# Kernel tuning notes

Measured on AMD Instinct MI355X. Metric: run time of the kernel, lower is better.

Reference implementation:

```python
import jax, jax.numpy as jnp
import numpy as np

N_NODES = 100000
N_EDGES = 1600000
NFEAT, NHID, NCLASS = 128, 64, 16


def setup_inputs() -> dict:
    key = jax.random.key(0)
    ks = jax.random.split(key, 8)
    x = jax.random.normal(ks[0], (N_NODES, NFEAT), dtype=jnp.float32)
    src = jax.random.randint(ks[1], (N_EDGES,), 0, N_NODES, dtype=jnp.int32)
    dst = jax.random.randint(ks[2], (N_EDGES,), 0, N_NODES, dtype=jnp.int32)
    edge_weight = jax.random.uniform(ks[3], (N_EDGES,), dtype=jnp.float32)
    W1 = jax.random.normal(ks[4], (NFEAT, NHID), dtype=jnp.float32) / np.sqrt(NFEAT)
    b1 = jnp.zeros((NHID,), dtype=jnp.float32)
    W2 = jax.random.normal(ks[5], (NHID, NCLASS), dtype=jnp.float32) / np.sqrt(NHID)
    b2 = jnp.zeros((NCLASS,), dtype=jnp.float32)
    return {"x": x, "src": src, "dst": dst, "edge_weight": edge_weight,
            "W1": W1, "b1": b1, "W2": W2, "b2": b2}


def _spmm(src, dst, edge_weight, support):
    # out[i] = sum_{e: dst[e]==i} w[e] * support[src[e]]   (adj @ support)
    msgs = edge_weight[:, None] * support[src]  # [E, d]
    return jax.ops.segment_sum(msgs, dst, num_segments=N_NODES)


def reference(x, src, dst, edge_weight, W1, b1, W2, b2):
    # layer 1: dense projection then sparse aggregation, relu
    h = jax.nn.relu(_spmm(src, dst, edge_weight, x @ W1) + b1)  # [N, nhid]
    # layer 2: identity activation
    logits = _spmm(src, dst, edge_weight, h @ W2) + b2          # [N, nclass]
    return jax.nn.log_softmax(logits, axis=1)
```

## Files before the change

### kernel.cpp

```cpp
#include <hip/hip_runtime.h>

#define N_NODES 100000
#define N_EDGES 1600000
#define NFEAT 128
#define NHID 64
#define NCLASS 16

#define BSHIFT 7
#define BUCK_NODES 128
#define NBUCK ((N_NODES + BUCK_NODES - 1) >> BSHIFT)
#define ECAP 2560
#define EDGE_TILE 8192
#define NB_SCAT ((N_EDGES + EDGE_TILE - 1) / EDGE_TILE)
#define EPT 16
#define NB_GEMM ((N_NODES + 127) / 128)

#define HPAD 65

#define SCALE1 262144.0f
#define INV_SCALE1 (1.0f / 262144.0f)
#define SCALE2 131072.0f
#define INV_SCALE2 (1.0f / 131072.0f)

typedef __attribute__((ext_vector_type(8))) short short8;
typedef __attribute__((ext_vector_type(4))) float float4v;

__device__ __forceinline__ float bflo(unsigned int u) {
    return __uint_as_float(u << 16);
}
__device__ __forceinline__ float bfhi(unsigned int u) {
    return __uint_as_float(u & 0xFFFF0000u);
}
__device__ __forceinline__ unsigned short f2bf(float f) {
    unsigned int b = __float_as_uint(f);
    b += 0x7FFFu + ((b >> 16) & 1u);
    return (unsigned short)(b >> 16);
}
__device__ __forceinline__ int fx(float v, float scale) {
    return __float2int_rn(v * scale);
}

__global__ __launch_bounds__(512) void k_gemm1_scatter(
        const float* __restrict__ x, const float* __restrict__ W1,
        unsigned short* __restrict__ s1,
        const int* __restrict__ dst, const int* __restrict__ src,
        const float* __restrict__ ew,
        int* __restrict__ fill, int2* __restrict__ edgeA) {
    __shared__ unsigned short w1t[64][136];
    __shared__ int hist[NBUCK], bbase[NBUCK], bfill[NBUCK];

    if (blockIdx.x >= NB_GEMM) {
        for (int i = threadIdx.x; i < NBUCK; i += 512) { hist[i] = 0; bfill[i] = 0; }

        const int bid  = blockIdx.x - NB_GEMM;
        const int base = bid * EDGE_TILE;
        int   d[EPT]; int s[EPT]; float w[EPT]; bool v[EPT];
#pragma unroll
        for (int k = 0; k < EPT; ++k) {
            int e = base + threadIdx.x + k * 512;
            v[k] = e < N_EDGES;
            d[k] = v[k] ? dst[e] : 0;
        }
#pragma unroll
        for (int k = 0; k < EPT; ++k) {
            int e = base + threadIdx.x + k * 512;
            s[k] = v[k] ? src[e] : 0;
        }
#pragma unroll
        for (int k = 0; k < EPT; ++k) {
            int e = base + threadIdx.x + k * 512;
            w[k] = v[k] ? ew[e] : 0.f;
        }
        __syncthreads();

#pragma unroll
        for (int k = 0; k < EPT; ++k)
            if (v[k]) atomicAdd(&hist[d[k] >> BSHIFT], 1);
        __syncthreads();

        {
            int rot = (bid * 53) % NBUCK;
            for (int i = threadIdx.x; i < NBUCK; i += 512) {
                int j = i + rot;
                if (j >= NBUCK) j -= NBUCK;
                bbase[j] = hist[j] ? atomicAdd(&fill[j], hist[j]) : 0;
            }
        }
        __syncthreads();

#pragma unroll
        for (int k = 0; k < EPT; ++k) {
            if (v[k]) {
                int bb = d[k] >> BSHIFT;
                int r  = bbase[bb] + atomicAdd(&bfill[bb], 1);
                if (r < ECAP)
                    edgeA[(size_t)bb * ECAP + r] =
                        make_int2(s[k] | ((d[k] & (BUCK_NODES - 1)) << 17),
                                  __float_as_int(w[k]));
            }
        }
        return;
    }

    for (int i = threadIdx.x; i < NFEAT * NHID; i += 512) {
        int n = i & 63, k = i >> 6;
        w1t[n][k] = f2bf(W1[k * NHID + n]);
    }
    __syncthreads();

    const int lane = threadIdx.x & 63;
    const int wv   = threadIdx.x >> 6;
    const int m    = lane & 15;
    const int quad = lane >> 4;
    const int node0 = blockIdx.x * 128 + wv * 16;
    if (node0 >= N_NODES) return;

    short8 bfrag[4][4];
#pragma unroll
    for (int kt = 0; kt < 4; ++kt)
#pragma unroll
        for (int nt = 0; nt < 4; ++nt)
            bfrag[kt][nt] = *(const short8*)&w1t[nt * 16 + m][kt * 32 + quad * 8];

    const float4* xr = (const float4*)(x + (size_t)node0 * NFEAT);
    float4v acc[4] = {{0.f,0.f,0.f,0.f},{0.f,0.f,0.f,0.f},
                      {0.f,0.f,0.f,0.f},{0.f,0.f,0.f,0.f}};
#pragma unroll
    for (int kt = 0; kt < 4; ++kt) {
        float4 f0 = xr[m * 32 + kt * 8 + quad * 2];
        float4 f1 = xr[m * 32 + kt * 8 + quad * 2 + 1];
        short8 a;
        a[0] = (short)f2bf(f0.x); a[1] = (short)f2bf(f0.y);
        a[2] = (short)f2bf(f0.z); a[3] = (short)f2bf(f0.w);
        a[4] = (short)f2bf(f1.x); a[5] = (short)f2bf(f1.y);
        a[6] = (short)f2bf(f1.z); a[7] = (short)f2bf(f1.w);
#pragma unroll
        for (int nt = 0; nt < 4; ++nt)
            acc[nt] = __builtin_amdgcn_mfma_f32_16x16x32_bf16(
                a, bfrag[kt][nt], acc[nt], 0, 0, 0);
    }
#pragma unroll
    for (int nt = 0; nt < 4; ++nt)
#pragma unroll
        for (int i = 0; i < 4; ++i)
            s1[(size_t)(node0 + quad * 4 + i) * NHID + nt * 16 + m] =
                f2bf(acc[nt][i]);
}

__global__ __launch_bounds__(512) void k_bagg1(const int* __restrict__ cnt,
                                               const int2* __restrict__ edgeA,
                                               const unsigned short* __restrict__ s1,
                                               const float* __restrict__ b1,
                                               const float* __restrict__ W2,
                                               unsigned short* __restrict__ s2) {
    __shared__ int h[BUCK_NODES][HPAD];
    const int b = blockIdx.x;
    for (int i = threadIdx.x; i < BUCK_NODES * HPAD; i += 512)
        ((int*)h)[i] = 0;
    __syncthreads();

    const int beg = b * ECAP;
    int c = cnt[b]; if (c > ECAP) c = ECAP;
    const int end = beg + c;
    const uint4* __restrict__ s1u4 = (const uint4*)s1;
    const int sg = threadIdx.x >> 3;
    const int r  = threadIdx.x & 7;
    const int f0 = r * 8;

    int p = beg + sg;
    for (; p + 192 < end; p += 256) {
        int2 e0 = edgeA[p], e1 = edgeA[p + 64], e2 = edgeA[p + 128], e3 = edgeA[p + 192];
        uint4 u0 = s1u4[(size_t)(e0.x & 0x1FFFF) * 8 + r];
        uint4 u1 = s1u4[(size_t)(e1.x & 0x1FFFF) * 8 + r];
        uint4 u2 = s1u4[(size_t)(e2.x & 0x1FFFF) * 8 + r];
        uint4 u3 = s1u4[(size_t)(e3.x & 0x1FFFF) * 8 + r];
        float w0 = __int_as_float(e0.y), w1 = __int_as_float(e1.y);
        float w2 = __int_as_float(e2.y), w3 = __int_as_float(e3.y);
        int* h0 = &h[e0.x >> 17][f0];
        int* h1 = &h[e1.x >> 17][f0];
        int* h2 = &h[e2.x >> 17][f0];
        int* h3 = &h[e3.x >> 17][f0];
        atomicAdd(h0 + 0, fx(w0 * bflo(u0.x), SCALE1)); atomicAdd(h0 + 1, fx(w0 * bfhi(u0.x), SCALE1));
        atomicAdd(h0 + 2, fx(w0 * bflo(u0.y), SCALE1)); atomicAdd(h0 + 3, fx(w0 * bfhi(u0.y), SCALE1));
        atomicAdd(h0 + 4, fx(w0 * bflo(u0.z), SCALE1)); atomicAdd(h0 + 5, fx(w0 * bfhi(u0.z), SCALE1));
        atomicAdd(h0 + 6, fx(w0 * bflo(u0.w), SCALE1)); atomicAdd(h0 + 7, fx(w0 * bfhi(u0.w), SCALE1));
        atomicAdd(h1 + 0, fx(w1 * bflo(u1.x), SCALE1)); atomicAdd(h1 + 1, fx(w1 * bfhi(u1.x), SCALE1));
        atomicAdd(h1 + 2, fx(w1 * bflo(u1.y), SCALE1)); atomicAdd(h1 + 3, fx(w1 * bfhi(u1.y), SCALE1));
        atomicAdd(h1 + 4, fx(w1 * bflo(u1.z), SCALE1)); atomicAdd(h1 + 5, fx(w1 * bfhi(u1.z), SCALE1));
        atomicAdd(h1 + 6, fx(w1 * bflo(u1.w), SCALE1)); atomicAdd(h1 + 7, fx(w1 * bfhi(u1.w), SCALE1));
        atomicAdd(h2 + 0, fx(w2 * bflo(u2.x), SCALE1)); atomicAdd(h2 + 1, fx(w2 * bfhi(u2.x), SCALE1));
        atomicAdd(h2 + 2, fx(w2 * bflo(u2.y), SCALE1)); atomicAdd(h2 + 3, fx(w2 * bfhi(u2.y), SCALE1));
        atomicAdd(h2 + 4, fx(w2 * bflo(u2.z), SCALE1)); atomicAdd(h2 + 5, fx(w2 * bfhi(u2.z), SCALE1));
        atomicAdd(h2 + 6, fx(w2 * bflo(u2.w), SCALE1)); atomicAdd(h2 + 7, fx(w2 * bfhi(u2.w), SCALE1));
        atomicAdd(h3 + 0, fx(w3 * bflo(u3.x), SCALE1)); atomicAdd(h3 + 1, fx(w3 * bfhi(u3.x), SCALE1));
        atomicAdd(h3 + 2, fx(w3 * bflo(u3.y), SCALE1)); atomicAdd(h3 + 3, fx(w3 * bfhi(u3.y), SCALE1));
        atomicAdd(h3 + 4, fx(w3 * bflo(u3.z), SCALE1)); atomicAdd(h3 + 5, fx(w3 * bfhi(u3.z), SCALE1));
        atomicAdd(h3 + 6, fx(w3 * bflo(u3.w), SCALE1)); atomicAdd(h3 + 7, fx(w3 * bfhi(u3.w), SCALE1));
    }
    for (; p < end; p += 64) {
        int2 e = edgeA[p];
        uint4 u = s1u4[(size_t)(e.x & 0x1FFFF) * 8 + r];
        float w = __int_as_float(e.y);
        int* hr = &h[e.x >> 17][f0];
        atomicAdd(hr + 0, fx(w * bflo(u.x), SCALE1)); atomicAdd(hr + 1, fx(w * bfhi(u.x), SCALE1));
        atomicAdd(hr + 2, fx(w * bflo(u.y), SCALE1)); atomicAdd(hr + 3, fx(w * bfhi(u.y), SCALE1));
        atomicAdd(hr + 4, fx(w * bflo(u.z), SCALE1)); atomicAdd(hr + 5, fx(w * bfhi(u.z), SCALE1));
        atomicAdd(hr + 6, fx(w * bflo(u.w), SCALE1)); atomicAdd(hr + 7, fx(w * bfhi(u.w), SCALE1));
    }
    __syncthreads();

    const int wv   = threadIdx.x >> 6;
    const int lane = threadIdx.x & 63;
    const int m    = lane & 15;
    const int quad = lane >> 4;
    const int node0 = b << BSHIFT;

    short8 bfr[2];
    float  b1v[2][8];
#pragma unroll
    for (int kt = 0; kt < 2; ++kt)
#pragma unroll
        for (int j = 0; j < 8; ++j) {
            int k = kt * 32 + quad * 8 + j;
            bfr[kt][j] = (short)f2bf(W2[k * NCLASS + m]);
            b1v[kt][j] = b1[k];
        }
    {
        const int row = wv * 16 + m;
        float4v acc = {0.f, 0.f, 0.f, 0.f};
#pragma unroll
        for (int kt = 0; kt < 2; ++kt) {
            short8 a;
#pragma unroll
            for (int j = 0; j < 8; ++j)
                a[j] = (short)f2bf(fmaxf(
                    (float)h[row][kt * 32 + quad * 8 + j] * INV_SCALE1 + b1v[kt][j],
                    0.f));
            acc = __builtin_amdgcn_mfma_f32_16x16x32_bf16(a, bfr[kt], acc, 0, 0, 0);
        }
        const int nr = node0 + wv * 16 + quad * 4;
#pragma unroll
        for (int i = 0; i < 4; ++i)
            if (nr + i < N_NODES)
                s2[(size_t)(nr + i) * NCLASS + m] = f2bf(acc[i]);
    }
}

__global__ __launch_bounds__(512) void k_bagg2(const int* __restrict__ cnt,
                                               const int2* __restrict__ edgeA,
                                               const unsigned short* __restrict__ s2,
                                               const float* __restrict__ b2,
                                               float* __restrict__ out) {
    __shared__ int h2[BUCK_NODES][17];
    const int b = blockIdx.x;
    for (int i = threadIdx.x; i < BUCK_NODES * 17; i += 512)
        ((int*)h2)[i] = 0;
    __syncthreads();

    const int beg = b * ECAP;
    int c = cnt[b]; if (c > ECAP) c = ECAP;
    const int end = beg + c;
    const unsigned int* __restrict__ s2u = (const unsigned int*)s2;
    const int sg = threadIdx.x >> 3;
    const int r  = threadIdx.x & 7;
    const int c0 = 2 * r;

    int p = beg + sg;
    for (; p + 192 < end; p += 256) {
        int2 e0 = edgeA[p], e1 = edgeA[p + 64], e2 = edgeA[p + 128], e3 = edgeA[p + 192];
        unsigned int u0 = s2u[(size_t)(e0.x & 0x1FFFF) * 8 + r];
        unsigned int u1 = s2u[(size_t)(e1.x & 0x1FFFF) * 8 + r];
        unsigned int u2 = s2u[(size_t)(e2.x & 0x1FFFF) * 8 + r];
        unsigned int u3 = s2u[(size_t)(e3.x & 0x1FFFF) * 8 + r];
        float w0 = __int_as_float(e0.y), w1 = __int_as_float(e1.y);
        float w2 = __int_as_float(e2.y), w3 = __int_as_float(e3.y);
        atomicAdd(&h2[e0.x >> 17][c0],     fx(w0 * bflo(u0), SCALE2));
        atomicAdd(&h2[e0.x >> 17][c0 + 1], fx(w0 * bfhi(u0), SCALE2));
        atomicAdd(&h2[e1.x >> 17][c0],     fx(w1 * bflo(u1), SCALE2));
        atomicAdd(&h2[e1.x >> 17][c0 + 1], fx(w1 * bfhi(u1), SCALE2));
        atomicAdd(&h2[e2.x >> 17][c0],     fx(w2 * bflo(u2), SCALE2));
        atomicAdd(&h2[e2.x >> 17][c0 + 1], fx(w2 * bfhi(u2), SCALE2));
        atomicAdd(&h2[e3.x >> 17][c0],     fx(w3 * bflo(u3), SCALE2));
        atomicAdd(&h2[e3.x >> 17][c0 + 1], fx(w3 * bfhi(u3), SCALE2));
    }
    for (; p < end; p += 64) {
        int2 e = edgeA[p];
        unsigned int u = s2u[(size_t)(e.x & 0x1FFFF) * 8 + r];
        float w = __int_as_float(e.y);
        atomicAdd(&h2[e.x >> 17][c0],     fx(w * bflo(u), SCALE2));
        atomicAdd(&h2[e.x >> 17][c0 + 1], fx(w * bfhi(u), SCALE2));
    }
    __syncthreads();

    if (threadIdx.x < BUCK_NODES) {
        const int n = (b << BSHIFT) + threadIdx.x;
        if (n < N_NODES) {
            float v[NCLASS];
            float mx = -1e30f;
#pragma unroll
            for (int cc = 0; cc < NCLASS; ++cc) {
                v[cc] = (float)h2[threadIdx.x][cc] * INV_SCALE2 + b2[cc];
                mx = fmaxf(mx, v[cc]);
            }
            float s = 0.f;
#pragma unroll
            for (int cc = 0; cc < NCLASS; ++cc) s += __expf(v[cc] - mx);
            float ls = mx + __logf(s);
            float* o = out + (size_t)n * NCLASS;
#pragma unroll
            for (int cc = 0; cc < NCLASS; cc += 4) {
                float4 o4 = make_float4(v[cc] - ls, v[cc + 1] - ls,
                                        v[cc + 2] - ls, v[cc + 3] - ls);
                *(float4*)(o + cc) = o4;
            }
        }
    }
}

extern "C" void kernel_launch(void* const* d_in, const int* in_sizes, int n_in,
                              void* d_out, int out_size, void* d_ws, size_t ws_size,
                              hipStream_t stream) {
    const float* x   = (const float*)d_in[0];
    const int*   src = (const int*)d_in[1];
    const int*   dst = (const int*)d_in[2];
    const float* ew  = (const float*)d_in[3];
    const float* W1  = (const float*)d_in[4];
    const float* b1  = (const float*)d_in[5];
    const float* W2  = (const float*)d_in[6];
    const float* b2  = (const float*)d_in[7];
    float* out = (float*)d_out;

    unsigned short* s1 = (unsigned short*)d_ws;
    unsigned short* s2 = s1 + (size_t)N_NODES * NHID;
    int2* edgeA        = (int2*)(s2 + (size_t)N_NODES * NCLASS);
    int*  fill         = (int*)(edgeA + (size_t)NBUCK * ECAP);

    hipMemsetAsync(fill, 0, sizeof(int) * NBUCK, stream);

    k_gemm1_scatter<<<NB_GEMM + NB_SCAT, 512, 0, stream>>>(x, W1, s1, dst, src, ew,
                                                           fill, edgeA);
    k_bagg1<<<NBUCK, 512, 0, stream>>>(fill, edgeA, s1, b1, W2, s2);
    k_bagg2<<<NBUCK, 512, 0, stream>>>(fill, edgeA, s2, b2, out);
}
```

Before: 182.9 us.

## Pack two biased fixed-point accumulators into 64-bit LDS atomics

Each fixed-point contribution gets a positive bias so it is non-negative, which lets two 32-bit lanes be added with a single 64-bit LDS atomicAdd without borrows crossing between halves. A per-node edge counter is added and used to subtract the accumulated bias after aggregation. This halves the number of LDS atomic operations in both aggregation kernels. The cost is an extra counter atomic per edge and row padding changes for 8-byte alignment, plus a risk of overflow in the low half if the biased sums exceed 32 bits.

```diff
diff --git a/kernel.cpp b/kernel.cpp
--- a/kernel.cpp
+++ b/kernel.cpp
@@ -15,15 +15,19 @@
 #define EPT 16
 #define NB_GEMM ((N_NODES + 127) / 128)
 
-#define HPAD 65
+#define HPAD 66
 
 #define SCALE1 262144.0f
 #define INV_SCALE1 (1.0f / 262144.0f)
 #define SCALE2 131072.0f
 #define INV_SCALE2 (1.0f / 131072.0f)
 
+#define BIASF 4194304.0f
+#define BIASSH 22
+
 typedef __attribute__((ext_vector_type(8))) short short8;
 typedef __attribute__((ext_vector_type(4))) float float4v;
+typedef unsigned long long u64t;
 
 __device__ __forceinline__ float bflo(unsigned int u) {
     return __uint_as_float(u << 16);
@@ -36,8 +40,18 @@
     b += 0x7FFFu + ((b >> 16) & 1u);
     return (unsigned short)(b >> 16);
 }
-__device__ __forceinline__ int fx(float v, float scale) {
-    return __float2int_rn(v * scale);
+__device__ __forceinline__ unsigned int fxb(float ws, float bf) {
+    return (unsigned int)__float2int_rn(fmaf(ws, bf, BIASF));
+}
+__device__ __forceinline__ void pk2(u64t* hp, unsigned int lo, unsigned int hi) {
+    atomicAdd(hp, ((u64t)hi << 32) | (u64t)lo);
+}
+__device__ __forceinline__ void pkadd8(int* hrow_f0, uint4 u, float ws) {
+    u64t* hp = (u64t*)hrow_f0;
+    pk2(hp + 0, fxb(ws, bflo(u.x)), fxb(ws, bfhi(u.x)));
+    pk2(hp + 1, fxb(ws, bflo(u.y)), fxb(ws, bfhi(u.y)));
+    pk2(hp + 2, fxb(ws, bflo(u.z)), fxb(ws, bfhi(u.z)));
+    pk2(hp + 3, fxb(ws, bflo(u.w)), fxb(ws, bfhi(u.w)));
 }
 
 __global__ __launch_bounds__(512) void k_gemm1_scatter(
@@ -174,38 +188,29 @@
         uint4 u1 = s1u4[(size_t)(e1.x & 0x1FFFF) * 8 + r];
         uint4 u2 = s1u4[(size_t)(e2.x & 0x1FFFF) * 8 + r];
         uint4 u3 = s1u4[(size_t)(e3.x & 0x1FFFF) * 8 + r];
-        float w0 = __int_as_float(e0.y), w1 = __int_as_float(e1.y);
-        float w2 = __int_as_float(e2.y), w3 = __int_as_float(e3.y);
-        int* h0 = &h[e0.x >> 17][f0];
-        int* h1 = &h[e1.x >> 17][f0];
-        int* h2 = &h[e2.x >> 17][f0];
-        int* h3 = &h[e3.x >> 17][f0];
-        atomicAdd(h0 + 0, fx(w0 * bflo(u0.x), SCALE1)); atomicAdd(h0 + 1, fx(w0 * bfhi(u0.x), SCALE1));
-        atomicAdd(h0 + 2, fx(w0 * bflo(u0.y), SCALE1)); atomicAdd(h0 + 3, fx(w0 * bfhi(u0.y), SCALE1));
-        atomicAdd(h0 + 4, fx(w0 * bflo(u0.z), SCALE1)); atomicAdd(h0 + 5, fx(w0 * bfhi(u0.z), SCALE1));
-        atomicAdd(h0 + 6, fx(w0 * bflo(u0.w), SCALE1)); atomicAdd(h0 + 7, fx(w0 * bfhi(u0.w), SCALE1));
-        atomicAdd(h1 + 0, fx(w1 * bflo(u1.x), SCALE1)); atomicAdd(h1 + 1, fx(w1 * bfhi(u1.x), SCALE1));
-        atomicAdd(h1 + 2, fx(w1 * bflo(u1.y), SCALE1)); atomicAdd(h1 + 3, fx(w1 * bfhi(u1.y), SCALE1));
-        atomicAdd(h1 + 4, fx(w1 * bflo(u1.z), SCALE1)); atomicAdd(h1 + 5, fx(w1 * bfhi(u1.z), SCALE1));
-        atomicAdd(h1 + 6, fx(w1 * bflo(u1.w), SCALE1)); atomicAdd(h1 + 7, fx(w1 * bfhi(u1.w), SCALE1));
-        atomicAdd(h2 + 0, fx(w2 * bflo(u2.x), SCALE1)); atomicAdd(h2 + 1, fx(w2 * bfhi(u2.x), SCALE1));
-        atomicAdd(h2 + 2, fx(w2 * bflo(u2.y), SCALE1)); atomicAdd(h2 + 3, fx(w2 * bfhi(u2.y), SCALE1));
-        atomicAdd(h2 + 4, fx(w2 * bflo(u2.z), SCALE1)); atomicAdd(h2 + 5, fx(w2 * bfhi(u2.z), SCALE1));
-        atomicAdd(h2 + 6, fx(w2 * bflo(u2.w), SCALE1)); atomicAdd(h2 + 7, fx(w2 * bfhi(u2.w), SCALE1));
-        atomicAdd(h3 + 0, fx(w3 * bflo(u3.x), SCALE1)); atomicAdd(h3 + 1, fx(w3 * bfhi(u3.x), SCALE1));
-        atomicAdd(h3 + 2, fx(w3 * bflo(u3.y), SCALE1)); atomicAdd(h3 + 3, fx(w3 * bfhi(u3.y), SCALE1));
-        atomicAdd(h3 + 4, fx(w3 * bflo(u3.z), SCALE1)); atomicAdd(h3 + 5, fx(w3 * bfhi(u3.z), SCALE1));
-        atomicAdd(h3 + 6, fx(w3 * bflo(u3.w), SCALE1)); atomicAdd(h3 + 7, fx(w3 * bfhi(u3.w), SCALE1));
+        float ws0 = __int_as_float(e0.y) * SCALE1;
+        float ws1 = __int_as_float(e1.y) * SCALE1;
+        float ws2 = __int_as_float(e2.y) * SCALE1;
+        float ws3 = __int_as_float(e3.y) * SCALE1;
+        int ld0 = e0.x >> 17, ld1 = e1.x >> 17, ld2 = e2.x >> 17, ld3 = e3.x >> 17;
+        pkadd8(&h[ld0][f0], u0, ws0);
+        pkadd8(&h[ld1][f0], u1, ws1);
+        pkadd8(&h[ld2][f0], u2, ws2);
+        pkadd8(&h[ld3][f0], u3, ws3);
+        if (r == 0) {
+            atomicAdd(&h[ld0][64], 1);
+            atomicAdd(&h[ld1][64], 1);
+            atomicAdd(&h[ld2][64], 1);
+            atomicAdd(&h[ld3][64], 1);
+        }
     }
     for (; p < end; p += 64) {
         int2 e = edgeA[p];
         uint4 u = s1u4[(size_t)(e.x & 0x1FFFF) * 8 + r];
-        float w = __int_as_float(e.y);
-        int* hr = &h[e.x >> 17][f0];
-        atomicAdd(hr + 0, fx(w * bflo(u.x), SCALE1)); atomicAdd(hr + 1, fx(w * bfhi(u.x), SCALE1));
-        atomicAdd(hr + 2, fx(w * bflo(u.y), SCALE1)); atomicAdd(hr + 3, fx(w * bfhi(u.y), SCALE1));
-        atomicAdd(hr + 4, fx(w * bflo(u.z), SCALE1)); atomicAdd(hr + 5, fx(w * bfhi(u.z), SCALE1));
-        atomicAdd(hr + 6, fx(w * bflo(u.w), SCALE1)); atomicAdd(hr + 7, fx(w * bfhi(u.w), SCALE1));
+        float ws = __int_as_float(e.y) * SCALE1;
+        int ld = e.x >> 17;
+        pkadd8(&h[ld][f0], u, ws);
+        if (r == 0) atomicAdd(&h[ld][64], 1);
     }
     __syncthreads();
 
@@ -227,15 +232,16 @@
         }
     {
         const int row = wv * 16 + m;
+        const unsigned int db = ((unsigned int)h[row][64]) << BIASSH;
         float4v acc = {0.f, 0.f, 0.f, 0.f};
 #pragma unroll
         for (int kt = 0; kt < 2; ++kt) {
             short8 a;
 #pragma unroll
-            for (int j = 0; j < 8; ++j)
-                a[j] = (short)f2bf(fmaxf(
-                    (float)h[row][kt * 32 + quad * 8 + j] * INV_SCALE1 + b1v[kt][j],
-                    0.f));
+            for (int j = 0; j < 8; ++j) {
+                int val = (int)((unsigned int)h[row][kt * 32 + quad * 8 + j] - db);
+                a[j] = (short)f2bf(fmaxf((float)val * INV_SCALE1 + b1v[kt][j], 0.f));
+            }
             acc = __builtin_amdgcn_mfma_f32_16x16x32_bf16(a, bfr[kt], acc, 0, 0, 0);
         }
         const int nr = node0 + wv * 16 + quad * 4;
@@ -251,9 +257,9 @@
                                                const unsigned short* __restrict__ s2,
                                                const float* __restrict__ b2,
                                                float* __restrict__ out) {
-    __shared__ int h2[BUCK_NODES][17];
+    __shared__ int h2[BUCK_NODES][18];
     const int b = blockIdx.x;
-    for (int i = threadIdx.x; i < BUCK_NODES * 17; i += 512)
+    for (int i = threadIdx.x; i < BUCK_NODES * 18; i += 512)
         ((int*)h2)[i] = 0;
     __syncthreads();
 
@@ -263,7 +269,6 @@
     const unsigned int* __restrict__ s2u = (const unsigned int*)s2;
     const int sg = threadIdx.x >> 3;
     const int r  = threadIdx.x & 7;
-    const int c0 = 2 * r;
 
     int p = beg + sg;
     for (; p + 192 < end; p += 256) {
@@ -272,34 +277,42 @@
         unsigned int u1 = s2u[(size_t)(e1.x & 0x1FFFF) * 8 + r];
         unsigned int u2 = s2u[(size_t)(e2.x & 0x1FFFF) * 8 + r];
         unsigned int u3 = s2u[(size_t)(e3.x & 0x1FFFF) * 8 + r];
-        float w0 = __int_as_float(e0.y), w1 = __int_as_float(e1.y);
-        float w2 = __int_as_float(e2.y), w3 = __int_as_float(e3.y);
-        atomicAdd(&h2[e0.x >> 17][c0],     fx(w0 * bflo(u0), SCALE2));
-        atomicAdd(&h2[e0.x >> 17][c0 + 1], fx(w0 * bfhi(u0), SCALE2));
-        atomicAdd(&h2[e1.x >> 17][c0],     fx(w1 * bflo(u1), SCALE2));
-        atomicAdd(&h2[e1.x >> 17][c0 + 1], fx(w1 * bfhi(u1), SCALE2));
-        atomicAdd(&h2[e2.x >> 17][c0],     fx(w2 * bflo(u2), SCALE2));
-        atomicAdd(&h2[e2.x >> 17][c0 + 1], fx(w2 * bfhi(u2), SCALE2));
-        atomicAdd(&h2[e3.x >> 17][c0],     fx(w3 * bflo(u3), SCALE2));
-        atomicAdd(&h2[e3.x >> 17][c0 + 1], fx(w3 * bfhi(u3), SCALE2));
+        float ws0 = __int_as_float(e0.y) * SCALE2;
+        float ws1 = __int_as_float(e1.y) * SCALE2;
+        float ws2 = __int_as_float(e2.y) * SCALE2;
+        float ws3 = __int_as_float(e3.y) * SCALE2;
+        int ld0 = e0.x >> 17, ld1 = e1.x >> 17, ld2 = e2.x >> 17, ld3 = e3.x >> 17;
+        pk2((u64t*)&h2[ld0][0] + r, fxb(ws0, bflo(u0)), fxb(ws0, bfhi(u0)));
+        pk2((u64t*)&h2[ld1][0] + r, fxb(ws1, bflo(u1)), fxb(ws1, bfhi(u1)));
+        pk2((u64t*)&h2[ld2][0] + r, fxb(ws2, bflo(u2)), fxb(ws2, bfhi(u2)));
+        pk2((u64t*)&h2[ld3][0] + r, fxb(ws3, bflo(u3)), fxb(ws3, bfhi(u3)));
+        if (r == 0) {
+            atomicAdd(&h2[ld0][16], 1);
+            atomicAdd(&h2[ld1][16], 1);
+            atomicAdd(&h2[ld2][16], 1);
+            atomicAdd(&h2[ld3][16], 1);
+        }
     }
     for (; p < end; p += 64) {
         int2 e = edgeA[p];
         unsigned int u = s2u[(size_t)(e.x & 0x1FFFF) * 8 + r];
-        float w = __int_as_float(e.y);
-        atomicAdd(&h2[e.x >> 17][c0],     fx(w * bflo(u), SCALE2));
-        atomicAdd(&h2[e.x >> 17][c0 + 1], fx(w * bfhi(u), SCALE2));
+        float ws = __int_as_float(e.y) * SCALE2;
+        int ld = e.x >> 17;
+        pk2((u64t*)&h2[ld][0] + r, fxb(ws, bflo(u)), fxb(ws, bfhi(u)));
+        if (r == 0) atomicAdd(&h2[ld][16], 1);
     }
     __syncthreads();
 
     if (threadIdx.x < BUCK_NODES) {
         const int n = (b << BSHIFT) + threadIdx.x;
         if (n < N_NODES) {
+            const unsigned int db = ((unsigned int)h2[threadIdx.x][16]) << BIASSH;
             float v[NCLASS];
             float mx = -1e30f;
 #pragma unroll
             for (int cc = 0; cc < NCLASS; ++cc) {
-                v[cc] = (float)h2[threadIdx.x][cc] * INV_SCALE2 + b2[cc];
+                int val = (int)((unsigned int)h2[threadIdx.x][cc] - db);
+                v[cc] = (float)val * INV_SCALE2 + b2[cc];
                 mx = fmaxf(mx, v[cc]);
             }
             float s = 0.f;
```

After: 183.0 us. About the same (+0.1%).
